# Optimization experiments

Measured on AMD Instinct MI355X. Metric: run time of the kernel, lower is better.

The kernel has to match this reference:

```python
import jax, jax.numpy as jnp
import numpy as np

B, L, D, H, NB = 4, 1024, 512, 8, 128
HD = D // H
EPS = 1e-6


def rmsnorm(x, w):
    v = jnp.mean(x * x, axis=-1, keepdims=True)
    return x * jax.lax.rsqrt(v + EPS) * w


def setup_inputs() -> dict:
    key = jax.random.key(0)
    ks = jax.random.split(key, 9)
    hidden_states = jax.random.normal(ks[0], (B, L, D), dtype=jnp.float32)
    # sorted unix-like timestamps (int32 to avoid x64 requirement)
    timestamps = jnp.sort(jax.random.randint(ks[1], (B, L), 0, 1_000_000, dtype=jnp.int32), axis=1)
    # causal mask (True = attend)
    attention_mask = jnp.broadcast_to(jnp.tril(jnp.ones((L, L), dtype=bool)), (B, 1, L, L))
    w = lambda k, sh: jax.random.normal(k, sh, dtype=jnp.float32) * 0.02
    return {
        'hidden_states': hidden_states,
        'attention_mask': attention_mask,
        'timestamps': timestamps,
        'ln_w': jnp.ones((D,), jnp.float32),
        'attn_ln_w': jnp.ones((D,), jnp.float32),
        'wq': w(ks[2], (D, D)),
        'wk': w(ks[3], (D, D)),
        'wv': w(ks[4], (D, D)),
        'wu': w(ks[5], (D, D)),
        'wo': w(ks[6], (D, D)),
        'ts_w': w(ks[7], (NB + 1,)),
        'pos_w': w(ks[8], (2 * L - 1,)),
    }


def rel_attn_bias(timestamps, ts_w, pos_w):
    # relative position bias: bias_pos[i, j] = pos_w[(L-1) + j - i]
    i = jnp.arange(L)
    idx = (L - 1) + i[None, :] - i[:, None]  # [L, L]
    pos_bias = pos_w[idx]  # [L, L]
    # bucketized relative time bias (HSTU): diff[b,i,j] = ext[b,i+1] - ext[b,j]
    ext = jnp.concatenate([timestamps, timestamps[:, -1:]], axis=1)  # [B, L+1]
    diff = ext[:, 1:, None] - ext[:, None, :-1]  # [B, L, L]
    logd = jnp.log(jnp.clip(jnp.abs(diff).astype(jnp.float32), 1.0, None)) / 0.301
    bucket = jnp.clip(logd.astype(jnp.int32), 0, NB)  # floor via int cast (logd >= 0)
    ts_bias = ts_w[bucket]  # [B, L, L]
    return ts_bias + pos_bias[None]  # [B, L, L]


def reference(hidden_states, attention_mask, timestamps, ln_w, attn_ln_w, wq, wk, wv, wu, wo, ts_w, pos_w):
    residual = hidden_states
    h = rmsnorm(hidden_states, ln_w)  # [B, L, D]
    q = jax.nn.silu(h @ wq.T).reshape(B, L, H, HD)
    k = jax.nn.silu(h @ wk.T).reshape(B, L, H, HD)
    v = jax.nn.silu(h @ wv.T).reshape(B, L, H, HD)
    qk = jnp.einsum('bihd,bjhd->bhij', q, k)  # [B, H, L, L]
    qk = qk + rel_attn_bias(timestamps, ts_w, pos_w)[:, None]  # broadcast over heads
    attn = jax.nn.silu(qk) / L
    attn = attn * attention_mask.astype(attn.dtype)
    attn_out = jnp.einsum('bhij,bjhd->bihd', attn, v).reshape(B, L, D)
    u = jax.nn.silu(h @ wu.T)
    gated = u * rmsnorm(attn_out, attn_ln_w)
    out = residual + gated @ wo.T
    return out, attn
```

## Files before the change

kernel.cpp:

```cpp
#include <hip/hip_runtime.h>
#include <hip/hip_bf16.h>

typedef __hip_bfloat16 bf16;
typedef __attribute__((ext_vector_type(8))) short short8;
typedef __attribute__((ext_vector_type(4))) float f32x4;

#define SL 1024
#define DIM 512
#define NH 8
#define HD 64
#define NBUCK 128

__device__ __forceinline__ float silu_f(float x) { return x / (1.0f + __expf(-x)); }

__device__ __forceinline__ short f2bf(float x) {
  bf16 b = __float2bfloat16(x);
  return *reinterpret_cast<short*>(&b);
}

__device__ __forceinline__ void gld_lds16(const void* g, void* l) {
  __builtin_amdgcn_global_load_lds(
      (const __attribute__((address_space(1))) void*)g,
      (__attribute__((address_space(3))) void*)l, 16, 0, 0);
}

__global__ void convert_w_k(const float* __restrict__ s0, const float* __restrict__ s1,
                            const float* __restrict__ s2, const float* __restrict__ s3,
                            const float* __restrict__ s4, bf16* __restrict__ dst) {
  int wsel = blockIdx.y;
  const float* src = wsel == 0 ? s0 : wsel == 1 ? s1 : wsel == 2 ? s2 : wsel == 3 ? s3 : s4;
  int i = (blockIdx.x * 256 + threadIdx.x) * 4;
  float4 v = *(const float4*)(src + i);
  bf16* d = dst + (size_t)wsel * DIM * DIM + i;
  d[0] = __float2bfloat16(v.x);
  d[1] = __float2bfloat16(v.y);
  d[2] = __float2bfloat16(v.z);
  d[3] = __float2bfloat16(v.w);
}

__global__ void rmsnorm_k(const float* __restrict__ x, const float* __restrict__ w,
                          bf16* __restrict__ out) {
  int row = blockIdx.x, l = threadIdx.x;
  const float4* xr = (const float4*)(x + (size_t)row * DIM);
  float4 v0 = xr[l], v1 = xr[l + 64];
  float s = v0.x*v0.x + v0.y*v0.y + v0.z*v0.z + v0.w*v0.w
          + v1.x*v1.x + v1.y*v1.y + v1.z*v1.z + v1.w*v1.w;
  #pragma unroll
  for (int o = 32; o; o >>= 1) s += __shfl_xor(s, o);
  float sc = rsqrtf(s * (1.0f / DIM) + 1e-6f);
  bf16* orow = out + (size_t)row * DIM;
  int c0 = l * 4, c1 = 256 + l * 4;
  orow[c0 + 0] = __float2bfloat16(v0.x * sc * w[c0 + 0]);
  orow[c0 + 1] = __float2bfloat16(v0.y * sc * w[c0 + 1]);
  orow[c0 + 2] = __float2bfloat16(v0.z * sc * w[c0 + 2]);
  orow[c0 + 3] = __float2bfloat16(v0.w * sc * w[c0 + 3]);
  orow[c1 + 0] = __float2bfloat16(v1.x * sc * w[c1 + 0]);
  orow[c1 + 1] = __float2bfloat16(v1.y * sc * w[c1 + 1]);
  orow[c1 + 2] = __float2bfloat16(v1.z * sc * w[c1 + 2]);
  orow[c1 + 3] = __float2bfloat16(v1.w * sc * w[c1 + 3]);
}

__device__ __forceinline__ void gemm128_core(const bf16* __restrict__ A,
                                             const bf16* __restrict__ Bt,
                                             short* lds, int bm, int bn,
                                             f32x4 acc[4][4]) {
  int t = threadIdx.x, w = t >> 6, l = t & 63;
  int ln = l & 15, g8 = (l >> 4) * 8;
  int wr = (w >> 1) * 64, wc = (w & 1) * 64;
  for (int kt = 0; kt < 16; ++kt) {
    if (kt) __syncthreads();
    #pragma unroll
    for (int i = 0; i < 4; ++i) {
      int s = i * 4 + w;
      int row = s * 16 + (l >> 2);
      int col = kt * 32 + (l & 3) * 8;
      const bf16* gsrc = (s < 8)
          ? (A  + (size_t)(bm * 128 + row) * DIM + col)
          : (Bt + (size_t)(bn * 128 + row - 128) * DIM + col);
      gld_lds16(gsrc, lds + s * 512 + l * 8);
    }
    __syncthreads();
    short8 a[4], b[4];
    #pragma unroll
    for (int m = 0; m < 4; ++m)
      a[m] = *(const short8*)(lds + (wr + m * 16 + ln) * 32 + g8);
    #pragma unroll
    for (int n = 0; n < 4; ++n)
      b[n] = *(const short8*)(lds + 4096 + (wc + n * 16 + ln) * 32 + g8);
    #pragma unroll
    for (int m = 0; m < 4; ++m)
      #pragma unroll
      for (int n = 0; n < 4; ++n)
        acc[m][n] = __builtin_amdgcn_mfma_f32_16x16x32_bf16(a[m], b[n], acc[m][n], 0, 0, 0);
  }
}

__global__ __launch_bounds__(256) void gemm_qkvu_k(const bf16* __restrict__ hb,
                                                   const bf16* __restrict__ wb,
                                                   bf16* __restrict__ q, bf16* __restrict__ k,
                                                   bf16* __restrict__ v, bf16* __restrict__ u) {
  __shared__ __align__(16) short lds[8192];
  int mode = blockIdx.y;
  int bm = blockIdx.x >> 2, bn = blockIdx.x & 3;
  f32x4 acc[4][4];
  #pragma unroll
  for (int m = 0; m < 4; ++m)
    #pragma unroll
    for (int n = 0; n < 4; ++n) { f32x4 z = {0.f, 0.f, 0.f, 0.f}; acc[m][n] = z; }
  gemm128_core(hb, wb + (size_t)mode * DIM * DIM, lds, bm, bn, acc);

  int t = threadIdx.x, w = t >> 6, l = t & 63;
  int ln = l & 15, l4 = (l >> 4) * 4;
  int wr = (w >> 1) * 64, wc = (w & 1) * 64;
  bf16* qkv = mode == 0 ? q : mode == 1 ? k : v;
  #pragma unroll
  for (int m = 0; m < 4; ++m)
    #pragma unroll
    for (int n = 0; n < 4; ++n)
      #pragma unroll
      for (int j = 0; j < 4; ++j) {
        int rg = bm * 128 + wr + m * 16 + l4 + j;
        int cg = bn * 128 + wc + n * 16 + ln;
        bf16 val = __float2bfloat16(silu_f(acc[m][n][j]));
        int b = rg >> 10, li = rg & 1023, hh = cg >> 6, dd = cg & 63;
        if (mode <= 2) qkv[((size_t)(b * NH + hh) * SL + li) * HD + dd] = val;
        else           u[(size_t)rg * DIM + cg] = val;
      }
}

__global__ __launch_bounds__(256) void transpose_v_k(const bf16* __restrict__ v,
                                                     bf16* __restrict__ vT) {
  int bh = blockIdx.y, t0 = blockIdx.x * 64;
  int t = threadIdx.x;
  __shared__ short ldsT[64 * 65];
  const bf16* vb = v + (size_t)bh * SL * HD;
  bf16* vtb = vT + (size_t)bh * HD * SL;
  int r = t >> 2, c = (t & 3) * 16;
  short8 x0 = *(const short8*)(vb + (size_t)(t0 + r) * HD + c);
  short8 x1 = *(const short8*)(vb + (size_t)(t0 + r) * HD + c + 8);
  #pragma unroll
  for (int qq = 0; qq < 8; ++qq) {
    ldsT[r * 65 + c + qq] = x0[qq];
    ldsT[r * 65 + c + 8 + qq] = x1[qq];
  }
  __syncthreads();
  int d = t >> 2, lc = (t & 3) * 16;
  short8 y0, y1;
  #pragma unroll
  for (int qq = 0; qq < 8; ++qq) {
    y0[qq] = ldsT[(lc + qq) * 65 + d];
    y1[qq] = ldsT[(lc + 8 + qq) * 65 + d];
  }
  bf16* dst = vtb + (size_t)d * SL + t0 + lc;
  *(short8*)dst = y0;
  *(short8*)(dst + 8) = y1;
}

__global__ __launch_bounds__(256) void qk_attn_k(const bf16* __restrict__ q,
                                                 const bf16* __restrict__ k,
                                                 const int* __restrict__ ts,
                                                 const float* __restrict__ ts_w,
                                                 const float* __restrict__ pos_w,
                                                 float* __restrict__ attn) {
  int bh = blockIdx.y, x = blockIdx.x;
  int ti = 0, accx = 0;
  while (accx + ti + 1 <= x) { accx += ti + 1; ++ti; }
  int tj = x - accx;
  int t = threadIdx.x, w = t >> 6, l = t & 63;
  int ln = l & 15, l4 = (l >> 4) * 4, g8 = (l >> 4) * 8;
  int wr = (w >> 1) * 64, wc = (w & 1) * 64;
  float* arow = attn + (size_t)bh * SL * SL;

  __shared__ __align__(16) short lds[16384];
  __shared__ float tw_l[NBUCK + 1];
  __shared__ float pw_l[255];
  __shared__ int tsi_l[128], tsj_l[128];

  const int* tsb = ts + (size_t)(bh >> 3) * SL;
  if (t < NBUCK + 1) tw_l[t] = ts_w[t];
  if (t < 255) pw_l[t] = pos_w[896 + (tj - ti) * 128 + t];
  if (t < 128) tsi_l[t] = tsb[min(ti * 128 + t + 1, SL - 1)];
  else         tsj_l[t - 128] = tsb[tj * 128 + (t - 128)];

  #pragma unroll
  for (int i = 0; i < 8; ++i) {
    int s = i * 4 + w;
    int row = (s & 15) * 8 + (l >> 3);
    int col = (l & 7) * 8;
    const bf16* g = (s < 16)
        ? (q + (size_t)bh * SL * HD + (size_t)(ti * 128 + row) * HD + col)
        : (k + (size_t)bh * SL * HD + (size_t)(tj * 128 + row) * HD + col);
    gld_lds16(g, lds + s * 512 + l * 8);
  }
  __syncthreads();

  f32x4 acc[4][4];
  #pragma unroll
  for (int m = 0; m < 4; ++m)
    #pragma unroll
    for (int n = 0; n < 4; ++n) { f32x4 z = {0.f, 0.f, 0.f, 0.f}; acc[m][n] = z; }
  #pragma unroll
  for (int kk = 0; kk < 64; kk += 32) {
    short8 a[4], b[4];
    #pragma unroll
    for (int m = 0; m < 4; ++m)
      a[m] = *(const short8*)(lds + (wr + m * 16 + ln) * 64 + kk + g8);
    #pragma unroll
    for (int n = 0; n < 4; ++n)
      b[n] = *(const short8*)(lds + 8192 + (wc + n * 16 + ln) * 64 + kk + g8);
    #pragma unroll
    for (int m = 0; m < 4; ++m)
      #pragma unroll
      for (int n = 0; n < 4; ++n)
        acc[m][n] = __builtin_amdgcn_mfma_f32_16x16x32_bf16(a[m], b[n], acc[m][n], 0, 0, 0);
  }

  const float LSC = 2.30281455f;
  #pragma unroll
  for (int m = 0; m < 4; ++m)
    #pragma unroll
    for (int j = 0; j < 4; ++j) {
      int il = wr + m * 16 + l4 + j;
      int tsi = tsi_l[il];
      int i = ti * 128 + il;
      #pragma unroll
      for (int n = 0; n < 4; ++n) {
        int jl = wc + n * 16 + ln;
        int jj = tj * 128 + jl;
        float v = acc[m][n][j];
        int dt = tsi - tsj_l[jl];
        float adf = fmaxf(fabsf((float)dt), 1.0f);
        int bucket = (int)(__log2f(adf) * LSC);
        bucket = bucket < 0 ? 0 : (bucket > NBUCK ? NBUCK : bucket);
        float bias = tw_l[bucket] + pw_l[jl - il + 127];
        float o = (jj <= i) ? silu_f(v + bias) * (1.0f / (float)SL) : 0.0f;
        arow[(size_t)i * SL + jj] = o;
      }
    }

  if (x < 28) {
    int zi = 0, acc2 = 0;
    while (acc2 + (7 - zi) <= x) { acc2 += 7 - zi; ++zi; }
    int zj = zi + 1 + (x - acc2);
    float4 z4 = make_float4(0.f, 0.f, 0.f, 0.f);
    #pragma unroll
    for (int rep = 0; rep < 16; ++rep) {
      int flat = rep * 256 + t;
      int row = flat >> 5, c4 = flat & 31;
      *(float4*)(arow + (size_t)(zi * 128 + row) * SL + zj * 128 + c4 * 4) = z4;
    }
  }
}

__global__ __launch_bounds__(256) void pv_k(const float* __restrict__ attn,
                                            const bf16* __restrict__ vT,
                                            float* __restrict__ ao0,
                                            float* __restrict__ ao1) {
  int bh = blockIdx.y, bm = blockIdx.x, sp = blockIdx.z;
  int t = threadIdx.x, w = t >> 6, l = t & 63;
  int ln = l & 15, l4 = (l >> 4) * 4, g8 = (l >> 4) * 8;
  __shared__ __align__(16) short lds[6144];
  const float* arow = attn + (size_t)bh * SL * SL;
  const bf16* vrow = vT + (size_t)bh * HD * SL;
  f32x4 acc[2][4];
  #pragma unroll
  for (int m = 0; m < 2; ++m)
    #pragma unroll
    for (int n = 0; n < 4; ++n) { f32x4 z = {0.f, 0.f, 0.f, 0.f}; acc[m][n] = z; }

  int klo = sp * (bm + 1) * 2;
  int khi = (sp + 1) * (bm + 1) * 2;
  for (int kt = klo; kt < khi; ++kt) {
    if (kt > klo) __syncthreads();
    {
      int s = w * 2;
      #pragma unroll
      for (int ss = 0; ss < 2; ++ss, ++s) {
        int row = s * 16 + (l >> 2);
        int col = kt * 32 + (l & 3) * 8;
        const float* g = arow + (size_t)(bm * 128 + row) * SL + col;
        float4 f0 = *(const float4*)g;
        float4 f1 = *(const float4*)(g + 4);
        short8 vv;
        vv[0] = f2bf(f0.x); vv[1] = f2bf(f0.y); vv[2] = f2bf(f0.z); vv[3] = f2bf(f0.w);
        vv[4] = f2bf(f1.x); vv[5] = f2bf(f1.y); vv[6] = f2bf(f1.z); vv[7] = f2bf(f1.w);
        *(short8*)(lds + s * 512 + l * 8) = vv;
      }
    }
    {
      int s = 8 + w;
      int r2 = (s - 8) * 16 + (l >> 2);
      int col = kt * 32 + (l & 3) * 8;
      gld_lds16(vrow + (size_t)r2 * SL + col, lds + s * 512 + l * 8);
    }
    __syncthreads();
    short8 a[2], b[4];
    #pragma unroll
    for (int m = 0; m < 2; ++m)
      a[m] = *(const short8*)(lds + (w * 32 + m * 16 + ln) * 32 + g8);
    #pragma unroll
    for (int n = 0; n < 4; ++n)
      b[n] = *(const short8*)(lds + 4096 + (n * 16 + ln) * 32 + g8);
    #pragma unroll
    for (int m = 0; m < 2; ++m)
      #pragma unroll
      for (int n = 0; n < 4; ++n)
        acc[m][n] = __builtin_amdgcn_mfma_f32_16x16x32_bf16(a[m], b[n], acc[m][n], 0, 0, 0);
  }

  float* aop = sp == 0 ? ao0 : ao1;
  int b = bh >> 3, hh = bh & 7;
  #pragma unroll
  for (int m = 0; m < 2; ++m)
    #pragma unroll
    for (int n = 0; n < 4; ++n)
      #pragma unroll
      for (int j = 0; j < 4; ++j) {
        int i = bm * 128 + w * 32 + m * 16 + l4 + j;
        int dd = n * 16 + ln;
        aop[((size_t)(b * SL + i)) * DIM + hh * HD + dd] = acc[m][n][j];
      }
}

__global__ void gated_k(const float* __restrict__ ao0, const float* __restrict__ ao1,
                        const bf16* __restrict__ u,
                        const float* __restrict__ w, bf16* __restrict__ g) {
  int row = blockIdx.x, l = threadIdx.x;
  const float4* ar0 = (const float4*)(ao0 + (size_t)row * DIM);
  const float4* ar1 = (const float4*)(ao1 + (size_t)row * DIM);
  float4 p0 = ar0[l], p1 = ar1[l], p2 = ar0[l + 64], p3 = ar1[l + 64];
  float4 a0 = make_float4(p0.x + p1.x, p0.y + p1.y, p0.z + p1.z, p0.w + p1.w);
  float4 a1 = make_float4(p2.x + p3.x, p2.y + p3.y, p2.z + p3.z, p2.w + p3.w);
  float s = a0.x*a0.x + a0.y*a0.y + a0.z*a0.z + a0.w*a0.w
          + a1.x*a1.x + a1.y*a1.y + a1.z*a1.z + a1.w*a1.w;
  #pragma unroll
  for (int o = 32; o; o >>= 1) s += __shfl_xor(s, o);
  float sc = rsqrtf(s * (1.0f / DIM) + 1e-6f);
  const bf16* ur = u + (size_t)row * DIM;
  bf16* gr = g + (size_t)row * DIM;
  int c0 = l * 4, c1 = 256 + l * 4;
  gr[c0 + 0] = __float2bfloat16(__bfloat162float(ur[c0 + 0]) * a0.x * sc * w[c0 + 0]);
  gr[c0 + 1] = __float2bfloat16(__bfloat162float(ur[c0 + 1]) * a0.y * sc * w[c0 + 1]);
  gr[c0 + 2] = __float2bfloat16(__bfloat162float(ur[c0 + 2]) * a0.z * sc * w[c0 + 2]);
  gr[c0 + 3] = __float2bfloat16(__bfloat162float(ur[c0 + 3]) * a0.w * sc * w[c0 + 3]);
  gr[c1 + 0] = __float2bfloat16(__bfloat162float(ur[c1 + 0]) * a1.x * sc * w[c1 + 0]);
  gr[c1 + 1] = __float2bfloat16(__bfloat162float(ur[c1 + 1]) * a1.y * sc * w[c1 + 1]);
  gr[c1 + 2] = __float2bfloat16(__bfloat162float(ur[c1 + 2]) * a1.z * sc * w[c1 + 2]);
  gr[c1 + 3] = __float2bfloat16(__bfloat162float(ur[c1 + 3]) * a1.w * sc * w[c1 + 3]);
}

__global__ __launch_bounds__(256) void gemm_out_k(const bf16* __restrict__ gated,
                                                  const bf16* __restrict__ wob,
                                                  const float* __restrict__ residual,
                                                  float* __restrict__ out) {
  int bm = blockIdx.x >> 3, bn = blockIdx.x & 7;
  int t = threadIdx.x, w = t >> 6, l = t & 63;
  int ln = l & 15, l4 = (l >> 4) * 4, g8 = (l >> 4) * 8;
  __shared__ __align__(16) short lds[6144];
  f32x4 acc[2][4];
  #pragma unroll
  for (int m = 0; m < 2; ++m)
    #pragma unroll
    for (int n = 0; n < 4; ++n) { f32x4 z = {0.f, 0.f, 0.f, 0.f}; acc[m][n] = z; }

  for (int kt = 0; kt < 16; ++kt) {
    if (kt) __syncthreads();
    #pragma unroll
    for (int i = 0; i < 3; ++i) {
      int s = i * 4 + w;
      int col = kt * 32 + (l & 3) * 8;
      const bf16* g;
      if (s < 8) { int row = s * 16 + (l >> 2); g = gated + (size_t)(bm * 128 + row) * DIM + col; }
      else       { int r2 = (s - 8) * 16 + (l >> 2); g = wob + (size_t)(bn * 64 + r2) * DIM + col; }
      gld_lds16(g, lds + s * 512 + l * 8);
    }
    __syncthreads();
    short8 a[2], b[4];
    #pragma unroll
    for (int m = 0; m < 2; ++m)
      a[m] = *(const short8*)(lds + (w * 32 + m * 16 + ln) * 32 + g8);
    #pragma unroll
    for (int n = 0; n < 4; ++n)
      b[n] = *(const short8*)(lds + 4096 + (n * 16 + ln) * 32 + g8);
    #pragma unroll
    for (int m = 0; m < 2; ++m)
      #pragma unroll
      for (int n = 0; n < 4; ++n)
        acc[m][n] = __builtin_amdgcn_mfma_f32_16x16x32_bf16(a[m], b[n], acc[m][n], 0, 0, 0);
  }

  #pragma unroll
  for (int m = 0; m < 2; ++m)
    #pragma unroll
    for (int n = 0; n < 4; ++n)
      #pragma unroll
      for (int j = 0; j < 4; ++j) {
        int rg = bm * 128 + w * 32 + m * 16 + l4 + j;
        int cg = bn * 64 + n * 16 + ln;
        size_t idx = (size_t)rg * DIM + cg;
        out[idx] = acc[m][n][j] + residual[idx];
      }
}

extern "C" void kernel_launch(void* const* d_in, const int* in_sizes, int n_in,
                              void* d_out, int out_size, void* d_ws, size_t ws_size,
                              hipStream_t stream) {
  const float* hidden    = (const float*)d_in[0];
  const int*   ts        = (const int*)d_in[2];
  const float* ln_w      = (const float*)d_in[3];
  const float* attn_ln_w = (const float*)d_in[4];
  const float* wq        = (const float*)d_in[5];
  const float* wk        = (const float*)d_in[6];
  const float* wv        = (const float*)d_in[7];
  const float* wu        = (const float*)d_in[8];
  const float* wo        = (const float*)d_in[9];
  const float* ts_w      = (const float*)d_in[10];
  const float* pos_w     = (const float*)d_in[11];

  float* out  = (float*)d_out;
  float* attn = out + 2097152;

  bf16* wb    = (bf16*)d_ws;
  bf16* hb    = wb + 5 * DIM * DIM;
  bf16* q     = hb + 2097152;
  bf16* k     = q + 2097152;
  bf16* v     = k + 2097152;
  bf16* vT    = v + 2097152;
  bf16* u     = vT + 2097152;
  bf16* gated = u + 2097152;
  float* ao0  = (float*)(gated + 2097152);
  float* ao1  = ao0 + 2097152;

  convert_w_k<<<dim3(256, 5), 256, 0, stream>>>(wq, wk, wv, wu, wo, wb);
  rmsnorm_k<<<4096, 64, 0, stream>>>(hidden, ln_w, hb);
  gemm_qkvu_k<<<dim3(128, 4), 256, 0, stream>>>(hb, wb, q, k, v, u);
  transpose_v_k<<<dim3(16, 32), 256, 0, stream>>>(v, vT);
  qk_attn_k<<<dim3(36, 32), 256, 0, stream>>>(q, k, ts, ts_w, pos_w, attn);
  pv_k<<<dim3(8, 32, 2), 256, 0, stream>>>(attn, vT, ao0, ao1);
  gated_k<<<4096, 64, 0, stream>>>(ao0, ao1, u, attn_ln_w, gated);
  gemm_out_k<<<256, 256, 0, stream>>>(gated, wb + 4 * DIM * DIM, hidden, out);
}
```

Baseline: 122.1 us.

## Fuse QK-bias-silu and PV into one attention kernel with swizzled LDS

Merges the QK/bias/silu kernel and the PV kernel into a single kernel per (row-block, head, split). Each tile's scores are written to the global attn output and also kept as bf16 in LDS, where they feed the PV MFMA directly. This avoids re-reading the fp32 attention matrix from global memory and its bf16 conversion, and removes one launch. K and V tiles use XOR-swizzled LDS layouts to reduce bank conflicts. The cost is more LDS per block, serialized loads per key tile without double buffering, and a load imbalance between the two causal splits.

```diff
diff --git a/kernel.cpp b/kernel.cpp
--- a/kernel.cpp
+++ b/kernel.cpp
@@ -22,6 +22,13 @@
   __builtin_amdgcn_global_load_lds(
       (const __attribute__((address_space(1))) void*)g,
       (__attribute__((address_space(3))) void*)l, 16, 0, 0);
+}
+
+__device__ __forceinline__ int sw64(int row, int chunk) {
+  return row * 64 + (((chunk ^ row) & 7) << 3) + ((chunk & ~7) << 3);
+}
+__device__ __forceinline__ int sw128(int row, int chunk) {
+  return row * 128 + (((chunk ^ row) & 7) << 3) + ((chunk & ~7) << 3);
 }
 
 __global__ void convert_w_k(const float* __restrict__ s0, const float* __restrict__ s1,
@@ -156,159 +163,163 @@
   *(short8*)(dst + 8) = y1;
 }
 
-__global__ __launch_bounds__(256) void qk_attn_k(const bf16* __restrict__ q,
-                                                 const bf16* __restrict__ k,
-                                                 const int* __restrict__ ts,
-                                                 const float* __restrict__ ts_w,
-                                                 const float* __restrict__ pos_w,
-                                                 float* __restrict__ attn) {
-  int bh = blockIdx.y, x = blockIdx.x;
-  int ti = 0, accx = 0;
-  while (accx + ti + 1 <= x) { accx += ti + 1; ++ti; }
-  int tj = x - accx;
+__global__ __launch_bounds__(256) void attn_fused_k(
+    const bf16* __restrict__ q, const bf16* __restrict__ k,
+    const bf16* __restrict__ vT, const int* __restrict__ ts,
+    const float* __restrict__ ts_w, const float* __restrict__ pos_w,
+    float* __restrict__ attn, float* __restrict__ ao0, float* __restrict__ ao1) {
+  int bm = blockIdx.x, bh = blockIdx.y, z = blockIdx.z;
   int t = threadIdx.x, w = t >> 6, l = t & 63;
   int ln = l & 15, l4 = (l >> 4) * 4, g8 = (l >> 4) * 8;
   int wr = (w >> 1) * 64, wc = (w & 1) * 64;
-  float* arow = attn + (size_t)bh * SL * SL;
-
-  __shared__ __align__(16) short lds[16384];
+
+  __shared__ __align__(16) short Kl[8192];
+  __shared__ __align__(16) short Vl[8192];
+  __shared__ __align__(16) short Sl[16384];
   __shared__ float tw_l[NBUCK + 1];
   __shared__ float pw_l[255];
   __shared__ int tsi_l[128], tsj_l[128];
 
+  float* arow = attn + (size_t)bh * SL * SL;
+  const bf16* qg = q + (size_t)bh * SL * HD;
+  const bf16* kg = k + (size_t)bh * SL * HD;
+  const bf16* vg = vT + (size_t)bh * HD * SL;
   const int* tsb = ts + (size_t)(bh >> 3) * SL;
+
+  int f = bm * 2 + z;
+  #pragma unroll
+  for (int zt = 0; zt < 2; ++zt) {
+    int idx = f * 2 + zt;
+    if (idx < 28) {
+      int zi = 0, a2 = 0;
+      while (a2 + (7 - zi) <= idx) { a2 += 7 - zi; ++zi; }
+      int zj = zi + 1 + (idx - a2);
+      float4 z4 = make_float4(0.f, 0.f, 0.f, 0.f);
+      #pragma unroll
+      for (int rep = 0; rep < 16; ++rep) {
+        int flat = rep * 256 + t;
+        int row = flat >> 5, c4 = flat & 31;
+        *(float4*)(arow + (size_t)(zi * 128 + row) * SL + zj * 128 + c4 * 4) = z4;
+      }
+    }
+  }
+
   if (t < NBUCK + 1) tw_l[t] = ts_w[t];
-  if (t < 255) pw_l[t] = pos_w[896 + (tj - ti) * 128 + t];
-  if (t < 128) tsi_l[t] = tsb[min(ti * 128 + t + 1, SL - 1)];
-  else         tsj_l[t - 128] = tsb[tj * 128 + (t - 128)];
-
-  #pragma unroll
-  for (int i = 0; i < 8; ++i) {
-    int s = i * 4 + w;
-    int row = (s & 15) * 8 + (l >> 3);
-    int col = (l & 7) * 8;
-    const bf16* g = (s < 16)
-        ? (q + (size_t)bh * SL * HD + (size_t)(ti * 128 + row) * HD + col)
-        : (k + (size_t)bh * SL * HD + (size_t)(tj * 128 + row) * HD + col);
-    gld_lds16(g, lds + s * 512 + l * 8);
+  if (t >= 128) tsi_l[t - 128] = tsb[min(bm * 128 + (t - 128) + 1, SL - 1)];
+
+  int n0 = (bm + 2) >> 1;
+  int lo = z ? n0 : 0;
+  int hi = z ? (bm + 1) : n0;
+
+  short8 qa[4][2];
+  if (lo < hi) {
+    #pragma unroll
+    for (int m = 0; m < 4; ++m)
+      #pragma unroll
+      for (int kb = 0; kb < 2; ++kb)
+        qa[m][kb] = *(const short8*)(qg + (size_t)(bm * 128 + wr + m * 16 + ln) * HD + kb * 32 + g8);
+    #pragma unroll
+    for (int i = 0; i < 4; ++i) {
+      int s = i * 4 + w;
+      int rk = s * 8 + (l >> 3), ck = (l & 7) ^ (rk & 7);
+      gld_lds16(kg + (size_t)(lo * 128 + rk) * HD + ck * 8, Kl + s * 512 + l * 8);
+      int rv = s * 4 + (l >> 4), cv = (l & 15) ^ (rv & 7);
+      gld_lds16(vg + (size_t)rv * SL + lo * 128 + cv * 8, Vl + s * 512 + l * 8);
+    }
+    if (t < 128) {
+      tsj_l[t] = tsb[lo * 128 + t];
+      if (t < 127) pw_l[128 + t] = pos_w[896 + (lo - bm) * 128 + 128 + t];
+    } else {
+      pw_l[t - 128] = pos_w[896 + (lo - bm) * 128 + (t - 128)];
+    }
   }
   __syncthreads();
 
-  f32x4 acc[4][4];
-  #pragma unroll
-  for (int m = 0; m < 4; ++m)
-    #pragma unroll
-    for (int n = 0; n < 4; ++n) { f32x4 z = {0.f, 0.f, 0.f, 0.f}; acc[m][n] = z; }
-  #pragma unroll
-  for (int kk = 0; kk < 64; kk += 32) {
-    short8 a[4], b[4];
+  f32x4 apv[2][4];
+  #pragma unroll
+  for (int m = 0; m < 2; ++m)
+    #pragma unroll
+    for (int n = 0; n < 4; ++n) { f32x4 zz = {0.f, 0.f, 0.f, 0.f}; apv[m][n] = zz; }
+
+  const float LSC = 2.30281455f;
+  for (int kt = lo; kt < hi; ++kt) {
+    f32x4 acc[4][4];
     #pragma unroll
     for (int m = 0; m < 4; ++m)
-      a[m] = *(const short8*)(lds + (wr + m * 16 + ln) * 64 + kk + g8);
-    #pragma unroll
-    for (int n = 0; n < 4; ++n)
-      b[n] = *(const short8*)(lds + 8192 + (wc + n * 16 + ln) * 64 + kk + g8);
+      #pragma unroll
+      for (int n = 0; n < 4; ++n) { f32x4 zz = {0.f, 0.f, 0.f, 0.f}; acc[m][n] = zz; }
+    #pragma unroll
+    for (int kb = 0; kb < 2; ++kb) {
+      short8 b[4];
+      #pragma unroll
+      for (int n = 0; n < 4; ++n)
+        b[n] = *(const short8*)(Kl + sw64(wc + n * 16 + ln, kb * 4 + (l >> 4)));
+      #pragma unroll
+      for (int m = 0; m < 4; ++m)
+        #pragma unroll
+        for (int n = 0; n < 4; ++n)
+          acc[m][n] = __builtin_amdgcn_mfma_f32_16x16x32_bf16(qa[m][kb], b[n], acc[m][n], 0, 0, 0);
+    }
     #pragma unroll
     for (int m = 0; m < 4; ++m)
       #pragma unroll
+      for (int j = 0; j < 4; ++j) {
+        int il = wr + m * 16 + l4 + j;
+        int i = bm * 128 + il;
+        int tsi = tsi_l[il];
+        #pragma unroll
+        for (int n = 0; n < 4; ++n) {
+          int jl = wc + n * 16 + ln;
+          int jj = kt * 128 + jl;
+          float v = acc[m][n][j];
+          int dt = tsi - tsj_l[jl];
+          float adf = fmaxf(fabsf((float)dt), 1.0f);
+          int bucket = (int)(__log2f(adf) * LSC);
+          bucket = bucket < 0 ? 0 : (bucket > NBUCK ? NBUCK : bucket);
+          float bias = tw_l[bucket] + pw_l[jl - il + 127];
+          float o = (jj <= i) ? silu_f(v + bias) * (1.0f / (float)SL) : 0.0f;
+          arow[(size_t)i * SL + jj] = o;
+          Sl[sw128(il, jl >> 3) + (jl & 7)] = f2bf(o);
+        }
+      }
+    __syncthreads();
+    #pragma unroll
+    for (int kb = 0; kb < 4; ++kb) {
+      short8 a2[2], b2[4];
+      #pragma unroll
+      for (int m = 0; m < 2; ++m)
+        a2[m] = *(const short8*)(Sl + sw128(w * 32 + m * 16 + ln, kb * 4 + (l >> 4)));
+      #pragma unroll
       for (int n = 0; n < 4; ++n)
-        acc[m][n] = __builtin_amdgcn_mfma_f32_16x16x32_bf16(a[m], b[n], acc[m][n], 0, 0, 0);
-  }
-
-  const float LSC = 2.30281455f;
-  #pragma unroll
-  for (int m = 0; m < 4; ++m)
-    #pragma unroll
-    for (int j = 0; j < 4; ++j) {
-      int il = wr + m * 16 + l4 + j;
-      int tsi = tsi_l[il];
-      int i = ti * 128 + il;
-      #pragma unroll
-      for (int n = 0; n < 4; ++n) {
-        int jl = wc + n * 16 + ln;
-        int jj = tj * 128 + jl;
-        float v = acc[m][n][j];
-        int dt = tsi - tsj_l[jl];
-        float adf = fmaxf(fabsf((float)dt), 1.0f);
-        int bucket = (int)(__log2f(adf) * LSC);
-        bucket = bucket < 0 ? 0 : (bucket > NBUCK ? NBUCK : bucket);
-        float bias = tw_l[bucket] + pw_l[jl - il + 127];
-        float o = (jj <= i) ? silu_f(v + bias) * (1.0f / (float)SL) : 0.0f;
-        arow[(size_t)i * SL + jj] = o;
-      }
-    }
-
-  if (x < 28) {
-    int zi = 0, acc2 = 0;
-    while (acc2 + (7 - zi) <= x) { acc2 += 7 - zi; ++zi; }
-    int zj = zi + 1 + (x - acc2);
-    float4 z4 = make_float4(0.f, 0.f, 0.f, 0.f);
-    #pragma unroll
-    for (int rep = 0; rep < 16; ++rep) {
-      int flat = rep * 256 + t;
-      int row = flat >> 5, c4 = flat & 31;
-      *(float4*)(arow + (size_t)(zi * 128 + row) * SL + zj * 128 + c4 * 4) = z4;
-    }
-  }
-}
-
-__global__ __launch_bounds__(256) void pv_k(const float* __restrict__ attn,
-                                            const bf16* __restrict__ vT,
-                                            float* __restrict__ ao0,
-                                            float* __restrict__ ao1) {
-  int bh = blockIdx.y, bm = blockIdx.x, sp = blockIdx.z;
-  int t = threadIdx.x, w = t >> 6, l = t & 63;
-  int ln = l & 15, l4 = (l >> 4) * 4, g8 = (l >> 4) * 8;
-  __shared__ __align__(16) short lds[6144];
-  const float* arow = attn + (size_t)bh * SL * SL;
-  const bf16* vrow = vT + (size_t)bh * HD * SL;
-  f32x4 acc[2][4];
-  #pragma unroll
-  for (int m = 0; m < 2; ++m)
-    #pragma unroll
-    for (int n = 0; n < 4; ++n) { f32x4 z = {0.f, 0.f, 0.f, 0.f}; acc[m][n] = z; }
-
-  int klo = sp * (bm + 1) * 2;
-  int khi = (sp + 1) * (bm + 1) * 2;
-  for (int kt = klo; kt < khi; ++kt) {
-    if (kt > klo) __syncthreads();
-    {
-      int s = w * 2;
-      #pragma unroll
-      for (int ss = 0; ss < 2; ++ss, ++s) {
-        int row = s * 16 + (l >> 2);
-        int col = kt * 32 + (l & 3) * 8;
-        const float* g = arow + (size_t)(bm * 128 + row) * SL + col;
-        float4 f0 = *(const float4*)g;
-        float4 f1 = *(const float4*)(g + 4);
-        short8 vv;
-        vv[0] = f2bf(f0.x); vv[1] = f2bf(f0.y); vv[2] = f2bf(f0.z); vv[3] = f2bf(f0.w);
-        vv[4] = f2bf(f1.x); vv[5] = f2bf(f1.y); vv[6] = f2bf(f1.z); vv[7] = f2bf(f1.w);
-        *(short8*)(lds + s * 512 + l * 8) = vv;
-      }
-    }
-    {
-      int s = 8 + w;
-      int r2 = (s - 8) * 16 + (l >> 2);
-      int col = kt * 32 + (l & 3) * 8;
-      gld_lds16(vrow + (size_t)r2 * SL + col, lds + s * 512 + l * 8);
-    }
-    __syncthreads();
-    short8 a[2], b[4];
-    #pragma unroll
-    for (int m = 0; m < 2; ++m)
-      a[m] = *(const short8*)(lds + (w * 32 + m * 16 + ln) * 32 + g8);
-    #pragma unroll
-    for (int n = 0; n < 4; ++n)
-      b[n] = *(const short8*)(lds + 4096 + (n * 16 + ln) * 32 + g8);
-    #pragma unroll
-    for (int m = 0; m < 2; ++m)
-      #pragma unroll
-      for (int n = 0; n < 4; ++n)
-        acc[m][n] = __builtin_amdgcn_mfma_f32_16x16x32_bf16(a[m], b[n], acc[m][n], 0, 0, 0);
-  }
-
-  float* aop = sp == 0 ? ao0 : ao1;
+        b2[n] = *(const short8*)(Vl + sw128(n * 16 + ln, kb * 4 + (l >> 4)));
+      #pragma unroll
+      for (int m = 0; m < 2; ++m)
+        #pragma unroll
+        for (int n = 0; n < 4; ++n)
+          apv[m][n] = __builtin_amdgcn_mfma_f32_16x16x32_bf16(a2[m], b2[n], apv[m][n], 0, 0, 0);
+    }
+    if (kt + 1 < hi) {
+      __syncthreads();
+      int nk = kt + 1;
+      #pragma unroll
+      for (int i = 0; i < 4; ++i) {
+        int s = i * 4 + w;
+        int rk = s * 8 + (l >> 3), ck = (l & 7) ^ (rk & 7);
+        gld_lds16(kg + (size_t)(nk * 128 + rk) * HD + ck * 8, Kl + s * 512 + l * 8);
+        int rv = s * 4 + (l >> 4), cv = (l & 15) ^ (rv & 7);
+        gld_lds16(vg + (size_t)rv * SL + nk * 128 + cv * 8, Vl + s * 512 + l * 8);
+      }
+      if (t < 128) {
+        tsj_l[t] = tsb[nk * 128 + t];
+        if (t < 127) pw_l[128 + t] = pos_w[896 + (nk - bm) * 128 + 128 + t];
+      } else {
+        pw_l[t - 128] = pos_w[896 + (nk - bm) * 128 + (t - 128)];
+      }
+      __syncthreads();
+    }
+  }
+
+  float* aop = z ? ao1 : ao0;
   int b = bh >> 3, hh = bh & 7;
   #pragma unroll
   for (int m = 0; m < 2; ++m)
@@ -318,7 +329,7 @@
       for (int j = 0; j < 4; ++j) {
         int i = bm * 128 + w * 32 + m * 16 + l4 + j;
         int dd = n * 16 + ln;
-        aop[((size_t)(b * SL + i)) * DIM + hh * HD + dd] = acc[m][n][j];
+        aop[((size_t)(b * SL + i)) * DIM + hh * HD + dd] = apv[m][n][j];
       }
 }
 
@@ -435,8 +446,7 @@
   rmsnorm_k<<<4096, 64, 0, stream>>>(hidden, ln_w, hb);
   gemm_qkvu_k<<<dim3(128, 4), 256, 0, stream>>>(hb, wb, q, k, v, u);
   transpose_v_k<<<dim3(16, 32), 256, 0, stream>>>(v, vT);
-  qk_attn_k<<<dim3(36, 32), 256, 0, stream>>>(q, k, ts, ts_w, pos_w, attn);
-  pv_k<<<dim3(8, 32, 2), 256, 0, stream>>>(attn, vT, ao0, ao1);
+  attn_fused_k<<<dim3(8, 32, 2), 256, 0, stream>>>(q, k, vT, ts, ts_w, pos_w, attn, ao0, ao1);
   gated_k<<<4096, 64, 0, stream>>>(ao0, ao1, u, attn_ln_w, gated);
   gemm_out_k<<<256, 256, 0, stream>>>(gated, wb + 4 * DIM * DIM, hidden, out);
 }
```

After: 151.7 us. +24.2%, slower.
